# Kernel tuning notes

Hardware: AMD Instinct MI355X
Metric: run time of the kernel (lower is better)

## Reference

```python
import jax, jax.numpy as jnp
import numpy as np

HEADS = 16
DIM_HEAD = 64
SCALE = DIM_HEAD ** -0.5
MASK_VALUE = -jnp.finfo(jnp.float32).max


def setup_inputs() -> dict:
    key = jax.random.key(0)
    ks = jax.random.split(key, 6)
    b, n, dim = 2, 2048, 1024
    mem_len = 2048
    inner = HEADS * DIM_HEAD  # 1024
    return {
        "x": jax.random.normal(ks[0], (b, n, dim), jnp.float32),
        "mem_k": jax.random.normal(ks[1], (b, mem_len, inner), jnp.float32),
        "mem_v": jax.random.normal(ks[2], (b, mem_len, inner), jnp.float32),
        "pos_bias": jax.random.normal(ks[3], (HEADS, n, mem_len + n), jnp.float32) * 0.02,
        "Wq": jax.random.normal(ks[4], (dim, inner), jnp.float32) * (dim ** -0.5),
        "Wkv": jax.random.normal(ks[5], (dim, 2 * inner), jnp.float32) * (dim ** -0.5),
    }


def reference(x, mem_k, mem_v, pos_bias, Wq, Wkv):
    b, n, _ = x.shape
    # projections (note: original module returns before applying to_out)
    q = (x @ Wq) * SCALE                      # [b, n, h*d]
    k, v = jnp.split(x @ Wkv, 2, axis=-1)     # each [b, n, h*d]
    k = jnp.concatenate((mem_k, k), axis=1)   # [b, j, h*d]
    v = jnp.concatenate((mem_v, v), axis=1)

    def split_heads(t):
        return t.reshape(t.shape[0], t.shape[1], HEADS, DIM_HEAD).transpose(0, 2, 1, 3)

    q, k, v = map(split_heads, (q, k, v))     # [b, h, i/j, d]
    sim = jnp.einsum('bhid,bhjd->bhij', q, k)
    sim = sim + pos_bias[None]                # broadcast over batch
    i, j = sim.shape[-2:]
    # causal mask: triu with offset j - i + 1 is masked out
    causal_mask = jnp.triu(jnp.ones((i, j), dtype=bool), k=j - i + 1)
    sim = jnp.where(causal_mask[None, None], MASK_VALUE, sim)
    attn = jax.nn.softmax(sim, axis=-1)
    out = jnp.einsum('bhij,bhjd->bhid', attn, v)     # [b, h, i, d]
    out = out.transpose(0, 2, 1, 3).reshape(b, n, HEADS * DIM_HEAD)
    return out
```

## Files before the change

### kernel.cpp

```cpp
#include <hip/hip_runtime.h>
#include <hip/hip_bf16.h>
#include <cstdint>

#define B_     2
#define N_     2048
#define DIM_   1024
#define H_     16
#define DH_    64
#define MEM_   2048
#define JT_    4096
#define INNER_ 1024
#define SCALE_ 0.125f

typedef float f32x4 __attribute__((ext_vector_type(4)));
typedef short s16x8 __attribute__((ext_vector_type(8)));
typedef short s16x4 __attribute__((ext_vector_type(4)));

__device__ __forceinline__ short bf16_of(float f) {
    __hip_bfloat16 h = __float2bfloat16(f);
    return *(short*)&h;
}

__device__ __forceinline__ void gload16(const void* g, short* l) {
    __builtin_amdgcn_global_load_lds(
        (const __attribute__((address_space(1))) unsigned int*)g,
        (__attribute__((address_space(3))) unsigned int*)l, 16, 0, 0);
}

__global__ __launch_bounds__(256) void cast_x(
    const float* __restrict__ x, short* __restrict__ xb)
{
    const int total4 = B_ * N_ * DIM_ / 4;
    for (int idx = blockIdx.x * blockDim.x + threadIdx.x; idx < total4;
         idx += gridDim.x * blockDim.x) {
        float4 v = ((const float4*)x)[idx];
        s16x4 o;
        o[0] = bf16_of(v.x); o[1] = bf16_of(v.y);
        o[2] = bf16_of(v.z); o[3] = bf16_of(v.w);
        *(s16x4*)&xb[idx * 4] = o;
    }
}

__global__ __launch_bounds__(256) void cast_w(
    const float* __restrict__ Wq, const float* __restrict__ Wkv,
    short* __restrict__ Wt)
{
    const int kt = blockIdx.x;
    const int nt = blockIdx.y;
    __shared__ float tile[64][65];
    const int t = threadIdx.x;
    const int r = t >> 2, s4 = (t & 3) * 16;

    const int n0 = nt * 64;
    const float* src;
    int ldn, nc0;
    if (n0 < 1024) { src = Wq;  ldn = 1024; nc0 = n0; }
    else           { src = Wkv; ldn = 2048; nc0 = n0 - 1024; }
    const float scale = (n0 < 1024) ? SCALE_ : 1.0f;

#pragma unroll
    for (int kq = 0; kq < 4; ++kq) {
        float4 v = *(const float4*)&src[(size_t)(kt * 64 + r) * ldn + nc0 + s4 + kq * 4];
        tile[s4 + kq * 4 + 0][r] = v.x;
        tile[s4 + kq * 4 + 1][r] = v.y;
        tile[s4 + kq * 4 + 2][r] = v.z;
        tile[s4 + kq * 4 + 3][r] = v.w;
    }
    __syncthreads();
    short ov[16];
#pragma unroll
    for (int e = 0; e < 16; ++e) ov[e] = bf16_of(tile[r][s4 + e] * scale);
    short* dst = &Wt[(size_t)(n0 + r) * 1024 + kt * 64 + s4];
    *(s16x8*)&dst[0] = *(s16x8*)&ov[0];
    *(s16x8*)&dst[8] = *(s16x8*)&ov[8];
}

#define PLDC 152

__global__ __launch_bounds__(256) void mfma_proj(
    const short* __restrict__ Wt, const short* __restrict__ xb,
    short* __restrict__ qbuf, short* __restrict__ kbuf, short* __restrict__ vtbuf)
{
    const int bc = blockIdx.x;
    const int bi = blockIdx.y;
    const int tid = threadIdx.x;
    const int w = tid >> 6, lane = tid & 63, g = lane >> 4, li = lane & 15;
    const int wr = w >> 1, wc = w & 1;

    __shared__ short smem[128 * PLDC];
    short* A_lds = smem;
    short* B_lds = smem + 8192;

    f32x4 acc[4][4];
#pragma unroll
    for (int m = 0; m < 4; ++m)
#pragma unroll
        for (int n = 0; n < 4; ++n) acc[m][n] = f32x4{0.f, 0.f, 0.f, 0.f};

    const size_t arow0 = (size_t)bc * 128;
    const size_t brow0 = (size_t)bi * 128;

    for (int t = 0; t < 16; ++t) {
        __syncthreads();
#pragma unroll
        for (int u = 0; u < 4; ++u) {
            const int c = (w * 4 + u) * 64 + lane;
            const int row = c >> 3, q = c & 7;
            const int qs = q ^ (row & 7);
            gload16(&Wt[(arow0 + row) * 1024 + t * 64 + qs * 8],
                    &A_lds[(w * 4 + u) * 512 + lane * 8]);
            gload16(&xb[(brow0 + row) * 1024 + t * 64 + qs * 8],
                    &B_lds[(w * 4 + u) * 512 + lane * 8]);
        }
        __syncthreads();
#pragma unroll
        for (int kc = 0; kc < 2; ++kc) {
            s16x8 af[4], bf[4];
#pragma unroll
            for (int mt = 0; mt < 4; ++mt) {
                const int row = wr * 64 + mt * 16 + li;
                af[mt] = *(const s16x8*)&A_lds[row * 64 + ((kc * 4 + g) ^ (row & 7)) * 8];
            }
#pragma unroll
            for (int nt = 0; nt < 4; ++nt) {
                const int row = wc * 64 + nt * 16 + li;
                bf[nt] = *(const s16x8*)&B_lds[row * 64 + ((kc * 4 + g) ^ (row & 7)) * 8];
            }
#pragma unroll
            for (int mt = 0; mt < 4; ++mt)
#pragma unroll
                for (int nt = 0; nt < 4; ++nt)
                    acc[mt][nt] = __builtin_amdgcn_mfma_f32_16x16x32_bf16(af[mt], bf[nt], acc[mt][nt], 0, 0, 0);
        }
    }

    __syncthreads();
    const int c0 = bc * 128;
    const int i0g = bi * 128;
    const int b = i0g >> 11;
    const int ii0 = i0g & 2047;

    if (c0 < 2048) {
#pragma unroll
        for (int mt = 0; mt < 4; ++mt)
#pragma unroll
            for (int nt = 0; nt < 4; ++nt) {
                const int i_l = wc * 64 + nt * 16 + li;
                const int c_l = wr * 64 + mt * 16 + g * 4;
                s16x4 v4;
                v4[0] = bf16_of(acc[mt][nt][0]);
                v4[1] = bf16_of(acc[mt][nt][1]);
                v4[2] = bf16_of(acc[mt][nt][2]);
                v4[3] = bf16_of(acc[mt][nt][3]);
                *(s16x4*)&smem[i_l * PLDC + c_l] = v4;
            }
        __syncthreads();
        const bool isq = (c0 < 1024);
#pragma unroll
        for (int u = 0; u < 8; ++u) {
            const int ch = tid + u * 256;
            const int i_l = ch >> 4, seg = ch & 15;
            s16x8 v = *(const s16x8*)&smem[i_l * PLDC + seg * 8];
            const int cg = c0 + seg * 8;
            const int h = (cg >> 6) & 15;
            const int d = cg & 63;
            if (isq)
                *(s16x8*)&qbuf[(((size_t)(b * H_ + h)) * N_ + ii0 + i_l) * DH_ + d] = v;
            else
                *(s16x8*)&kbuf[(((size_t)(b * H_ + h)) * JT_ + MEM_ + ii0 + i_l) * DH_ + d] = v;
        }
    } else {
#pragma unroll
        for (int mt = 0; mt < 4; ++mt)
#pragma unroll
            for (int nt = 0; nt < 4; ++nt) {
                const int i_l = wc * 64 + nt * 16 + li;
                const int c_b = wr * 64 + mt * 16 + g * 4;
#pragma unroll
                for (int r = 0; r < 4; ++r)
                    smem[(c_b + r) * PLDC + i_l] = bf16_of(acc[mt][nt][r]);
            }
        __syncthreads();
#pragma unroll
        for (int u = 0; u < 8; ++u) {
            const int ch = tid + u * 256;
            const int c_l = ch >> 4, seg = ch & 15;
            s16x8 v = *(const s16x8*)&smem[c_l * PLDC + seg * 8];
            const int cv = c0 + c_l - 2048;
            const int h = cv >> 6, d = cv & 63;
            *(s16x8*)&vtbuf[(((size_t)(b * H_ + h)) * DH_ + d) * JT_ + MEM_ + ii0 + seg * 8] = v;
        }
    }
}

__global__ __launch_bounds__(256) void prep_mem(
    const float* __restrict__ mem_k, const float* __restrict__ mem_v,
    short* __restrict__ kbuf, short* __restrict__ vtbuf)
{
    const int jt = blockIdx.x, h = blockIdx.y;
    const int b = blockIdx.z & 1, task = blockIdx.z >> 1;
    const int j0 = jt * 64;
    const int t = threadIdx.x;
    const int r = t >> 2, s4 = (t & 3) * 16;
    const size_t bh = (size_t)(b * H_ + h);

    if (task == 0) {
        short ov[16];
#pragma unroll
        for (int k = 0; k < 4; ++k) {
            float4 v = *(const float4*)&mem_k[((size_t)(b * MEM_ + j0 + r)) * INNER_ + h * DH_ + s4 + k * 4];
            ov[k * 4 + 0] = bf16_of(v.x);
            ov[k * 4 + 1] = bf16_of(v.y);
            ov[k * 4 + 2] = bf16_of(v.z);
            ov[k * 4 + 3] = bf16_of(v.w);
        }
        short* dst = &kbuf[(bh * JT_ + j0 + r) * DH_ + s4];
        *(s16x8*)&dst[0] = *(s16x8*)&ov[0];
        *(s16x8*)&dst[8] = *(s16x8*)&ov[8];
    } else {
        __shared__ float tile[64][65];
#pragma unroll
        for (int k = 0; k < 4; ++k) {
            float4 v = *(const float4*)&mem_v[((size_t)(b * MEM_ + j0 + r)) * INNER_ + h * DH_ + s4 + k * 4];
            tile[s4 + k * 4 + 0][r] = v.x;
            tile[s4 + k * 4 + 1][r] = v.y;
            tile[s4 + k * 4 + 2][r] = v.z;
            tile[s4 + k * 4 + 3][r] = v.w;
        }
        __syncthreads();
        short ov[16];
#pragma unroll
        for (int e = 0; e < 16; ++e) ov[e] = bf16_of(tile[r][s4 + e]);
        short* dst = &vtbuf[(bh * DH_ + r) * JT_ + j0 + s4];
        *(s16x8*)&dst[0] = *(s16x8*)&ov[0];
        *(s16x8*)&dst[8] = *(s16x8*)&ov[8];
    }
}

__global__ __launch_bounds__(256, 4) void attn_flash(
    const short* __restrict__ qbuf, const short* __restrict__ kbuf,
    const short* __restrict__ vtbuf, const float* __restrict__ pos_bias,
    float* __restrict__ out)
{
    const int lid = blockIdx.x;
    const int h   = (lid & 7) | (((lid >> 3) & 1) << 3);
    const int b   = (lid >> 4) & 1;
    const int zql = (lid >> 5) & 15;
    const int hi  = lid >> 9;
    const int zq  = hi ? (31 - zql) : zql;
    const int i0  = zq * 64;

    const int tid = threadIdx.x;
    const int w = tid >> 6, lane = tid & 63, g = lane >> 4, li = lane & 15;

    __shared__ short K_lds[2][64 * 64];
    __shared__ short VT_lds[2][64 * 64];
    __shared__ short P_lds[4][16 * 64];

    const size_t bh = (size_t)(b * H_ + h);
    const short* kg  = kbuf  + bh * (size_t)JT_ * DH_;
    const short* vtg = vtbuf + bh * (size_t)DH_ * JT_;
    const float* pb  = pos_bias + (size_t)h * N_ * JT_;

    const int qw = i0 + w * 16;

    s16x8 aq[2];
#pragma unroll
    for (int kc = 0; kc < 2; ++kc)
        aq[kc] = *(const s16x8*)&qbuf[(bh * N_ + qw + li) * DH_ + kc * 32 + g * 8];

    f32x4 o[4];
    float m_run = -3.0e38f, l_run = 0.f;
#pragma unroll
    for (int dt = 0; dt < 4; ++dt) o[dt] = f32x4{0.f, 0.f, 0.f, 0.f};

    const int ntiles = 33 + zq;

    #define STAGE(bufi, j0s)                                                   \
    {                                                                          \
        _Pragma("unroll")                                                      \
        for (int u = 0; u < 2; ++u) {                                          \
            const int c = u * 256 + tid;                                       \
            const int row = c >> 3, q = c & 7;                                 \
            const int qs = q ^ (row & 7);                                      \
            gload16(&kg[(size_t)((j0s) + row) * DH_ + qs * 8],                 \
                    &K_lds[bufi][c * 8]);                                      \
            gload16(&vtg[(size_t)row * JT_ + (j0s) + qs * 8],                  \
                    &VT_lds[bufi][c * 8]);                                     \
        }                                                                      \
    }

    f32x4 bnext[4];
    #define LOADB(j0s)                                                         \
    {                                                                          \
        _Pragma("unroll")                                                      \
        for (int nt = 0; nt < 4; ++nt)                                         \
            bnext[nt] = *(const f32x4*)&pb[(size_t)(qw + li) * JT_ + (j0s) + nt * 16 + g * 4]; \
    }

    STAGE(0, 0);
    LOADB(0);
    __syncthreads();

    for (int t = 0; t < ntiles; ++t) {
        const int cur = t & 1;
        const int j0 = t * 64;
        const bool more = (t + 1 < ntiles);

        if (more) STAGE(cur ^ 1, j0 + 64);

        f32x4 sacc[4];
#pragma unroll
        for (int nt = 0; nt < 4; ++nt) sacc[nt] = bnext[nt];

        if (more) LOADB(j0 + 64);

        __builtin_amdgcn_s_setprio(1);
#pragma unroll
        for (int kc = 0; kc < 2; ++kc)
#pragma unroll
            for (int nt = 0; nt < 4; ++nt) {
                s16x8 bk = *(const s16x8*)&K_lds[cur][(nt * 16 + li) * 64 + ((kc * 4 + g) ^ (li & 7)) * 8];
                sacc[nt] = __builtin_amdgcn_mfma_f32_16x16x32_bf16(bk, aq[kc], sacc[nt], 0, 0, 0);
            }
        __builtin_amdgcn_s_setprio(0);

        const int q = qw + li;
        if (j0 + 63 > MEM_ + qw) {
#pragma unroll
            for (int nt = 0; nt < 4; ++nt)
#pragma unroll
                for (int r = 0; r < 4; ++r) {
                    const int jg = j0 + nt * 16 + g * 4 + r;
                    if (jg > MEM_ + q) sacc[nt][r] = -1e30f;
                }
        }

        float t0 = fmaxf(fmaxf(sacc[0][0], sacc[0][1]), fmaxf(sacc[0][2], sacc[0][3]));
        float t1 = fmaxf(fmaxf(sacc[1][0], sacc[1][1]), fmaxf(sacc[1][2], sacc[1][3]));
        float t2 = fmaxf(fmaxf(sacc[2][0], sacc[2][1]), fmaxf(sacc[2][2], sacc[2][3]));
        float t3 = fmaxf(fmaxf(sacc[3][0], sacc[3][1]), fmaxf(sacc[3][2], sacc[3][3]));
        float tml = fmaxf(fmaxf(t0, t1), fmaxf(t2, t3));
        if (!__all(tml <= m_run + 8.0f)) {
            float tm = tml;
            tm = fmaxf(tm, __shfl_xor(tm, 16));
            tm = fmaxf(tm, __shfl_xor(tm, 32));
            const float m_new = fmaxf(m_run, tm);
            const float sc = __expf(m_run - m_new);
            m_run = m_new;
            l_run *= sc;
#pragma unroll
            for (int dt = 0; dt < 4; ++dt) o[dt] *= sc;
        }

#pragma unroll
        for (int nt = 0; nt < 4; ++nt)
#pragma unroll
            for (int r = 0; r < 4; ++r)
                sacc[nt][r] = __expf(sacc[nt][r] - m_run);

        float s0 = (sacc[0][0] + sacc[0][1]) + (sacc[0][2] + sacc[0][3]);
        float s1 = (sacc[1][0] + sacc[1][1]) + (sacc[1][2] + sacc[1][3]);
        float s2 = (sacc[2][0] + sacc[2][1]) + (sacc[2][2] + sacc[2][3]);
        float s3 = (sacc[3][0] + sacc[3][1]) + (sacc[3][2] + sacc[3][3]);
        l_run += (s0 + s1) + (s2 + s3);

#pragma unroll
        for (int nt = 0; nt < 4; ++nt) {
            const int sl = nt * 4 + g;
            const int gi = (sl >> 1) ^ (li & 7);
            s16x4 pk;
            pk[0] = bf16_of(sacc[nt][0]);
            pk[1] = bf16_of(sacc[nt][1]);
            pk[2] = bf16_of(sacc[nt][2]);
            pk[3] = bf16_of(sacc[nt][3]);
            *(s16x4*)&P_lds[w][li * 64 + gi * 8 + (sl & 1) * 4] = pk;
        }

        __builtin_amdgcn_s_setprio(1);
#pragma unroll
        for (int kc = 0; kc < 2; ++kc) {
            const int gir = (kc * 4 + g) ^ (li & 7);
            s16x8 pf = *(const s16x8*)&P_lds[w][li * 64 + gir * 8];
#pragma unroll
            for (int dt = 0; dt < 4; ++dt) {
                s16x8 bv = *(const s16x8*)&VT_lds[cur][(dt * 16 + li) * 64 + ((kc * 4 + g) ^ (li & 7)) * 8];
                o[dt] = __builtin_amdgcn_mfma_f32_16x16x32_bf16(bv, pf, o[dt], 0, 0, 0);
            }
        }
        __builtin_amdgcn_s_setprio(0);

        __syncthreads();
    }
    #undef STAGE
    #undef LOADB

    {
        float ts = l_run;
        ts += __shfl_xor(ts, 16);
        ts += __shfl_xor(ts, 32);
        const float rinv = 1.0f / ts;
        const int q = qw + li;
#pragma unroll
        for (int dt = 0; dt < 4; ++dt) {
            f32x4 ov = o[dt] * rinv;
            *(f32x4*)&out[((size_t)(b * N_ + q)) * INNER_ + h * DH_ + dt * 16 + g * 4] = ov;
        }
    }
}

extern "C" void kernel_launch(void* const* d_in, const int* in_sizes, int n_in,
                              void* d_out, int out_size, void* d_ws, size_t ws_size,
                              hipStream_t stream)
{
    const float* x        = (const float*)d_in[0];
    const float* mem_k    = (const float*)d_in[1];
    const float* mem_v    = (const float*)d_in[2];
    const float* pos_bias = (const float*)d_in[3];
    const float* Wq       = (const float*)d_in[4];
    const float* Wkv      = (const float*)d_in[5];
    float* out = (float*)d_out;

    char* ws = (char*)d_ws;
    short* qbuf  = (short*)(ws);
    short* kbuf  = (short*)(ws + (8u << 20));
    short* vtbuf = (short*)(ws + (24u << 20));
    short* xb    = (short*)(ws + (40u << 20));
    short* Wt    = (short*)(ws + (48u << 20));

    cast_x<<<2048, 256, 0, stream>>>(x, xb);
    cast_w<<<dim3(16, 48), 256, 0, stream>>>(Wq, Wkv, Wt);
    prep_mem<<<dim3(32, H_, 4), 256, 0, stream>>>(mem_k, mem_v, kbuf, vtbuf);

    mfma_proj<<<dim3(24, 32), 256, 0, stream>>>(Wt, xb, qbuf, kbuf, vtbuf);

    attn_flash<<<1024, 256, 0, stream>>>(qbuf, kbuf, vtbuf, pos_bias, out);
}
```

Measured before the change: 226.8 us.

## Load K/V fragments directly from global into registers, drop shared-memory staging

New measurement: 492.8 us. +117.2%, slower.

```diff
diff --git a/kernel.cpp b/kernel.cpp
--- a/kernel.cpp
+++ b/kernel.cpp
@@ -237,7 +237,7 @@
     }
 }
 
-__global__ __launch_bounds__(256, 4) void attn_flash(
+__global__ __launch_bounds__(256, 3) void attn_flash(
     const short* __restrict__ qbuf, const short* __restrict__ kbuf,
     const short* __restrict__ vtbuf, const float* __restrict__ pos_bias,
     float* __restrict__ out)
@@ -253,8 +253,6 @@
     const int tid = threadIdx.x;
     const int w = tid >> 6, lane = tid & 63, g = lane >> 4, li = lane & 15;
 
-    __shared__ short K_lds[2][64 * 64];
-    __shared__ short VT_lds[2][64 * 64];
     __shared__ short P_lds[4][16 * 64];
 
     const size_t bh = (size_t)(b * H_ + h);
@@ -276,21 +274,26 @@
 
     const int ntiles = 33 + zq;
 
-    #define STAGE(bufi, j0s)                                                   \
+    s16x8 kf[2][4];
+    s16x8 vf[2][4];
+    f32x4 bnext[4];
+
+    #define LOADK(j0s)                                                         \
     {                                                                          \
         _Pragma("unroll")                                                      \
-        for (int u = 0; u < 2; ++u) {                                          \
-            const int c = u * 256 + tid;                                       \
-            const int row = c >> 3, q = c & 7;                                 \
-            const int qs = q ^ (row & 7);                                      \
-            gload16(&kg[(size_t)((j0s) + row) * DH_ + qs * 8],                 \
-                    &K_lds[bufi][c * 8]);                                      \
-            gload16(&vtg[(size_t)row * JT_ + (j0s) + qs * 8],                  \
-                    &VT_lds[bufi][c * 8]);                                     \
-        }                                                                      \
-    }
-
-    f32x4 bnext[4];
+        for (int kc = 0; kc < 2; ++kc)                                         \
+        _Pragma("unroll")                                                      \
+        for (int nt = 0; nt < 4; ++nt)                                         \
+            kf[kc][nt] = *(const s16x8*)&kg[(size_t)((j0s) + nt * 16 + li) * DH_ + kc * 32 + g * 8]; \
+    }
+    #define LOADV(j0s)                                                         \
+    {                                                                          \
+        _Pragma("unroll")                                                      \
+        for (int kc = 0; kc < 2; ++kc)                                         \
+        _Pragma("unroll")                                                      \
+        for (int dt = 0; dt < 4; ++dt)                                         \
+            vf[kc][dt] = *(const s16x8*)&vtg[(size_t)(dt * 16 + li) * JT_ + (j0s) + kc * 32 + g * 8]; \
+    }
     #define LOADB(j0s)                                                         \
     {                                                                          \
         _Pragma("unroll")                                                      \
@@ -298,17 +301,14 @@
             bnext[nt] = *(const f32x4*)&pb[(size_t)(qw + li) * JT_ + (j0s) + nt * 16 + g * 4]; \
     }
 
-    STAGE(0, 0);
+    LOADK(0);
+    LOADV(0);
     LOADB(0);
-    __syncthreads();
 
     for (int t = 0; t < ntiles; ++t) {
-        const int cur = t & 1;
         const int j0 = t * 64;
         const bool more = (t + 1 < ntiles);
 
-        if (more) STAGE(cur ^ 1, j0 + 64);
-
         f32x4 sacc[4];
 #pragma unroll
         for (int nt = 0; nt < 4; ++nt) sacc[nt] = bnext[nt];
@@ -319,11 +319,11 @@
 #pragma unroll
         for (int kc = 0; kc < 2; ++kc)
 #pragma unroll
-            for (int nt = 0; nt < 4; ++nt) {
-                s16x8 bk = *(const s16x8*)&K_lds[cur][(nt * 16 + li) * 64 + ((kc * 4 + g) ^ (li & 7)) * 8];
-                sacc[nt] = __builtin_amdgcn_mfma_f32_16x16x32_bf16(bk, aq[kc], sacc[nt], 0, 0, 0);
-            }
+            for (int nt = 0; nt < 4; ++nt)
+                sacc[nt] = __builtin_amdgcn_mfma_f32_16x16x32_bf16(kf[kc][nt], aq[kc], sacc[nt], 0, 0, 0);
         __builtin_amdgcn_s_setprio(0);
+
+        if (more) LOADK(j0 + 64);
 
         const int q = qw + li;
         if (j0 + 63 > MEM_ + qw) {
@@ -383,16 +383,15 @@
             const int gir = (kc * 4 + g) ^ (li & 7);
             s16x8 pf = *(const s16x8*)&P_lds[w][li * 64 + gir * 8];
 #pragma unroll
-            for (int dt = 0; dt < 4; ++dt) {
-                s16x8 bv = *(const s16x8*)&VT_lds[cur][(dt * 16 + li) * 64 + ((kc * 4 + g) ^ (li & 7)) * 8];
-                o[dt] = __builtin_amdgcn_mfma_f32_16x16x32_bf16(bv, pf, o[dt], 0, 0, 0);
-            }
+            for (int dt = 0; dt < 4; ++dt)
+                o[dt] = __builtin_amdgcn_mfma_f32_16x16x32_bf16(vf[kc][dt], pf, o[dt], 0, 0, 0);
         }
         __builtin_amdgcn_s_setprio(0);
 
-        __syncthreads();
-    }
-    #undef STAGE
+        if (more) LOADV(j0 + 64);
+    }
+    #undef LOADK
+    #undef LOADV
     #undef LOADB
 
     {
```
